# Performance work log

Measured on AMD Instinct MI355X. Metric: run time of the kernel, lower is better.

The kernel has to match this reference:

```python
import jax, jax.numpy as jnp
import numpy as np

GROUP_SIZE = 128
EPS = 1e-6
# AWQ nibble interleave order within each int32
_AWQ_SHIFTS = jnp.array([0, 4, 1, 5, 2, 6, 3, 7], dtype=jnp.uint32) * 4


def dequant_awq(qw, qz, sc, group_size=GROUP_SIZE):
    # qw: (in, out//8) int32, qz: (in//g, out//8) int32, sc: (in//g, out) float
    in_dim = qw.shape[0]
    w4 = ((qw.astype(jnp.uint32)[:, :, None] >> _AWQ_SHIFTS) & 0xF).astype(sc.dtype)
    z4 = ((qz.astype(jnp.uint32)[:, :, None] >> _AWQ_SHIFTS) & 0xF).astype(sc.dtype)
    w4 = w4.reshape(in_dim, -1)                    # (in, out)
    z4 = z4.reshape(qz.shape[0], -1)               # (in//g, out)
    z = jnp.repeat(z4, group_size, axis=0)         # (in, out)
    s = jnp.repeat(sc, group_size, axis=0)         # (in, out)
    return (w4 - z) * s


def rmsnorm(x, w, eps=EPS):
    return x * w * jax.lax.rsqrt(jnp.mean(x * x, axis=-1, keepdims=True) + eps)


def setup_inputs() -> dict:
    key = jax.random.key(0)
    ks = jax.random.split(key, 16)
    H, I, G = 2048, 8192, GROUP_SIZE
    IMAX = 2**31 - 1
    d = {}
    d['x'] = jax.random.normal(ks[0], (2, 2048, H), dtype=jnp.float32)
    d['ln1_w'] = jnp.ones((H,), jnp.float32)
    d['ln2_w'] = jnp.ones((H,), jnp.float32)
    d['qkv_qw'] = jax.random.randint(ks[1], (H, 3 * H // 8), 0, IMAX, dtype=jnp.int32)
    d['qkv_qz'] = jax.random.randint(ks[2], (H // G, 3 * H // 8), 0, IMAX, dtype=jnp.int32)
    d['qkv_sc'] = jax.random.normal(ks[3], (H // G, 3 * H), dtype=jnp.float32) * 0.02
    d['o_qw'] = jax.random.randint(ks[4], (H, H // 8), 0, IMAX, dtype=jnp.int32)
    d['o_qz'] = jax.random.randint(ks[5], (H // G, H // 8), 0, IMAX, dtype=jnp.int32)
    d['o_sc'] = jax.random.normal(ks[6], (H // G, H), dtype=jnp.float32) * 0.02
    d['gu_qw'] = jax.random.randint(ks[7], (H, 2 * I // 8), 0, IMAX, dtype=jnp.int32)
    d['gu_qz'] = jax.random.randint(ks[8], (H // G, 2 * I // 8), 0, IMAX, dtype=jnp.int32)
    d['gu_sc'] = jax.random.normal(ks[9], (H // G, 2 * I), dtype=jnp.float32) * 0.02
    d['dn_qw'] = jax.random.randint(ks[10], (I, H // 8), 0, IMAX, dtype=jnp.int32)
    d['dn_qz'] = jax.random.randint(ks[11], (I // G, H // 8), 0, IMAX, dtype=jnp.int32)
    d['dn_sc'] = jax.random.normal(ks[12], (I // G, H), dtype=jnp.float32) * 0.02
    return d


def reference(x, ln1_w, ln2_w, qkv_qw, qkv_qz, qkv_sc, o_qw, o_qz, o_sc,
              gu_qw, gu_qz, gu_sc, dn_qw, dn_qz, dn_sc):
    H = x.shape[-1]
    # attention-ish block (mock: qkv proj, take q slice, o proj)
    residual = x
    h = rmsnorm(x, ln1_w)
    qkv = h @ dequant_awq(qkv_qw, qkv_qz, qkv_sc)          # (..., 3H)
    q = qkv[..., :H]
    o = q @ dequant_awq(o_qw, o_qz, o_sc)                  # (..., H)
    x = residual + o
    # SwiGLU MLP
    residual = x
    h = rmsnorm(x, ln2_w)
    gate_up = h @ dequant_awq(gu_qw, gu_qz, gu_sc)         # (..., 2I)
    gate, up = jnp.split(gate_up, 2, axis=-1)
    mlp = (jax.nn.silu(gate) * up) @ dequant_awq(dn_qw, dn_qz, dn_sc)
    return residual + mlp
```

## Files before the change

kernel.cpp:

```cpp
#include <hip/hip_runtime.h>
#include <hip/hip_bf16.h>
#include <stdint.h>

typedef __bf16 bf16x8 __attribute__((ext_vector_type(8)));
typedef __bf16 bf16x2 __attribute__((ext_vector_type(2)));
typedef float  f32x4  __attribute__((ext_vector_type(4)));

template <int V> struct ic { static constexpr int value = V; };

__device__ __forceinline__ void gload_lds16(const void* g, void* l) {
  __builtin_amdgcn_global_load_lds(
      (const __attribute__((address_space(1))) void*)g,
      (__attribute__((address_space(3))) void*)l, 16, 0, 0);
}

__global__ __launch_bounds__(256) void rmsnorm_kernel(
    const float* __restrict__ x, const float* __restrict__ w,
    __bf16* __restrict__ out) {
  constexpr int H = 2048;
  const int row = blockIdx.x;
  const int t = threadIdx.x;
  const float4* xr = (const float4*)(x + (size_t)row * H);
  float4 a = xr[t * 2 + 0];
  float4 b = xr[t * 2 + 1];
  float ss = a.x*a.x + a.y*a.y + a.z*a.z + a.w*a.w
           + b.x*b.x + b.y*b.y + b.z*b.z + b.w*b.w;
#pragma unroll
  for (int o = 32; o > 0; o >>= 1) ss += __shfl_xor(ss, o);
  __shared__ float red[4];
  if ((t & 63) == 0) red[t >> 6] = ss;
  __syncthreads();
  float tot = red[0] + red[1] + red[2] + red[3];
  float r = rsqrtf(tot * (1.0f / H) + 1e-6f);
  const float4* wr4 = (const float4*)w;
  float4 wa = wr4[t * 2 + 0];
  float4 wb = wr4[t * 2 + 1];
  bf16x8 ov;
  ov[0] = (__bf16)(a.x * wa.x * r);
  ov[1] = (__bf16)(a.y * wa.y * r);
  ov[2] = (__bf16)(a.z * wa.z * r);
  ov[3] = (__bf16)(a.w * wa.w * r);
  ov[4] = (__bf16)(b.x * wb.x * r);
  ov[5] = (__bf16)(b.y * wb.y * r);
  ov[6] = (__bf16)(b.z * wb.z * r);
  ov[7] = (__bf16)(b.w * wb.w * r);
  *(bf16x8*)(out + (size_t)row * H + (size_t)t * 8) = ov;
}

template <int GU>
__global__ __launch_bounds__(256) void dequant_t_kernel(
    const int* __restrict__ qw, const int* __restrict__ qz,
    const float* __restrict__ sc, __bf16* __restrict__ wt,
    int K, int Cp, int Nfull) {
  const int t = threadIdx.x;
  const int k0 = blockIdx.x * 128 + (t & 63) * 2;
  const int c0 = blockIdx.y * 64 + (t >> 6) * 16;
  const int g = k0 >> 7;
  const uint32_t* qw0 = (const uint32_t*)qw + (size_t)k0 * Cp + c0;
  const uint32_t* qw1 = qw0 + Cp;
  const uint32_t* qzr = (const uint32_t*)qz + (size_t)g * Cp + c0;
  const float* scr = sc + (size_t)g * Nfull + (size_t)c0 * 8;

  uint32_t u0[16], u1[16], z[16];
#pragma unroll
  for (int j = 0; j < 4; j++) {
    *(int4*)(&u0[j*4]) = *(const int4*)(qw0 + j*4);
    *(int4*)(&u1[j*4]) = *(const int4*)(qw1 + j*4);
    *(int4*)(&z[j*4])  = *(const int4*)(qzr + j*4);
  }

#pragma unroll
  for (int i = 0; i < 16; i++) {
#pragma unroll
    for (int s = 0; s < 8; s++) {
      const int sh = ((s >> 1) * 4) + ((s & 1) ? 16 : 0);
      const float zf = (float)((z[i] >> sh) & 15u);
      const float scv = scr[i * 8 + s];
      const float w0 = ((float)((u0[i] >> sh) & 15u) - zf) * scv;
      const float w1 = ((float)((u1[i] >> sh) & 15u) - zf) * scv;
      const int n = (c0 + i) * 8 + s;
      int row;
      if (GU) row = (n < 8192) ? ((n >> 4) * 32 + (n & 15))
                               : (((n - 8192) >> 4) * 32 + 16 + (n & 15));
      else    row = n;
      bf16x2 pv = {(__bf16)w0, (__bf16)w1};
      *(bf16x2*)(wt + (size_t)row * K + k0) = pv;
    }
  }
}

template <int BN, int EPI, int KC>
__global__ __launch_bounds__(512, 2) void gemm8p_kernel(
    const __bf16* __restrict__ A, const __bf16* __restrict__ Bt,
    void* __restrict__ Cv, const float* __restrict__ addend,
    int M, int N) {
  constexpr int NT = KC / 64;
  constexpr int BQ = BN / 64;
  constexpr int NSTRIP = BN / 4;
  constexpr int NI = NSTRIP / 16;

  __shared__ alignas(16) __bf16 As[8 * 4096];
  __shared__ alignas(16) __bf16 Bs[2 * BQ * 4096];

  const int t = threadIdx.x;
  const int w = t >> 6, l = t & 63;
  const int lm = l & 15, kb = l >> 4;
  const int l7 = lm & 7;
  const int wm = w >> 2, wn = w & 3;

  const size_t stat = (size_t)(t >> 3) * KC + (size_t)(((t & 7) ^ ((t >> 3) & 7)) << 3);

  const int nwg = gridDim.x;
  const int bid = blockIdx.x;
  const int swz = (bid & 7) * (nwg >> 3) + (bid >> 3);
  const int nbm = M >> 8;
  const int per_g = nbm * 8;
  const int grp = swz / per_g, v = swz % per_g;
  const int bm0 = (v % nbm) * 256;
  const int bn0 = (grp * 8 + v / nbm) * BN;

  const __bf16* Ab = A + (size_t)bm0 * KC;
  const __bf16* Bb = Bt + (size_t)bn0 * KC;

  const uint32_t gsw0 = (uint32_t)((kb ^ l7) << 4);
  const uint32_t gsw1 = (uint32_t)(((4 + kb) ^ l7) << 4);
  const uint32_t arow = (uint32_t)(wm * 16384 + lm * 128);
  const uint32_t aoff0 = arow + gsw0, aoff1 = arow + gsw1;
  const uint32_t brow = (BN == 256)
      ? (uint32_t)(wn * 8192 + lm * 128)
      : (uint32_t)((wn >> 1) * 8192 + (wn & 1) * 4096 + lm * 128);
  const uint32_t boff0 = brow + gsw0, boff1 = brow + gsw1;
  const char* AsC = (const char*)As;
  const char* BsC = (const char*)Bs;

  f32x4 acc[8][NI] = {};
  bf16x8 af[2][2][2];
  bf16x8 bfr[2][NI][2];

  auto ldAf = [&](int dD, int mi, bf16x8* dst) {
    const uint32_t imA = (uint32_t)((dD * 4 + (mi >> 2)) * 8192 + (mi & 3) * 2048);
    dst[0] = *(const bf16x8*)(AsC + aoff0 + imA);
    dst[1] = *(const bf16x8*)(AsC + aoff1 + imA);
  };
  auto ldBf = [&](int dD) {
#pragma unroll
    for (int ni = 0; ni < NI; ++ni) {
      const uint32_t imB = (uint32_t)(dD * BQ * 8192 + ni * 2048);
      bfr[dD][ni][0] = *(const bf16x8*)(BsC + boff0 + imB);
      bfr[dD][ni][1] = *(const bf16x8*)(BsC + boff1 + imB);
    }
  };
  auto mfma4 = [&](int q, bf16x8 afq[2][2], int dD) {
    __builtin_amdgcn_s_setprio(1);
#pragma unroll
    for (int kk = 0; kk < 2; ++kk)
#pragma unroll
      for (int ni = 0; ni < NI; ++ni)
#pragma unroll
        for (int m2 = 0; m2 < 2; ++m2)
          acc[q * 2 + m2][ni] = __builtin_amdgcn_mfma_f32_16x16x32_bf16(
              afq[m2][kk], bfr[dD][ni][kk], acc[q * 2 + m2][ni], 0, 0, 0);
    __builtin_amdgcn_s_setprio(0);
  };

#pragma unroll
  for (int qa = 0; qa < 4; ++qa)
    gload_lds16(Ab + stat + (size_t)(qa * 64) * KC, As + qa * 4096 + t * 8);
#pragma unroll
  for (int qb = 0; qb < BQ; ++qb)
    gload_lds16(Bb + stat + (size_t)(qb * 64) * KC, Bs + qb * 4096 + t * 8);
#pragma unroll
  for (int qb = 0; qb < BQ; ++qb)
    gload_lds16(Bb + stat + (size_t)(qb * 64) * KC + 64, Bs + (BQ + qb) * 4096 + t * 8);
  gload_lds16(Ab + stat + 64, As + 4 * 4096 + t * 8);
  gload_lds16(Ab + stat + (size_t)128 * KC + 64, As + 6 * 4096 + t * 8);
  if (BN == 256) asm volatile("s_waitcnt vmcnt(6)" ::: "memory");
  else           asm volatile("s_waitcnt vmcnt(4)" ::: "memory");
  __builtin_amdgcn_s_barrier();

  ldAf(0, 0, af[0][0]); ldAf(0, 1, af[0][1]);
  ldBf(0);
  asm volatile("" ::: "memory");

  const __bf16* pA0 = Ab + stat + 128;
  const __bf16* pA1 = Ab + stat + (size_t)64 * KC + 64;
  const __bf16* pA2 = Ab + stat + (size_t)128 * KC + 128;
  const __bf16* pA3 = Ab + stat + (size_t)192 * KC + 64;
  const __bf16* pB0 = Bb + stat + 128;
  const __bf16* pB1 = Bb + stat + (size_t)64 * KC + 128;
  const __bf16* pB2 = Bb + stat + (size_t)128 * KC + 128;
  const __bf16* pB3 = Bb + stat + (size_t)192 * KC + 128;

  auto tile = [&](auto Dc, auto Sc) {
    constexpr int D = decltype(Dc)::value;
    constexpr int STG = decltype(Sc)::value;
    ldAf(D, 2, af[1][0]); ldAf(D, 3, af[1][1]);
    asm volatile("" ::: "memory");
    if (STG >= 1) {
      gload_lds16(pA1, As + ((D ^ 1) * 4 + 1) * 4096 + t * 8);
      gload_lds16(pA3, As + ((D ^ 1) * 4 + 3) * 4096 + t * 8);
    }
    __builtin_amdgcn_s_barrier();
    mfma4(0, af[0], D);
    __builtin_amdgcn_s_barrier();
    ldAf(D, 4, af[0][0]); ldAf(D, 5, af[0][1]);
    asm volatile("" ::: "memory");
    if (STG == 2) {
      gload_lds16(pB0, Bs + (D * BQ + 0) * 4096 + t * 8);
      gload_lds16(pB1, Bs + (D * BQ + 1) * 4096 + t * 8);
    }
    __builtin_amdgcn_s_barrier();
    mfma4(1, af[1], D);
    __builtin_amdgcn_s_barrier();
    ldAf(D, 6, af[1][0]); ldAf(D, 7, af[1][1]);
    asm volatile("" ::: "memory");
    if (STG == 2) {
      if (BN == 256) {
        gload_lds16(pB2, Bs + (D * BQ + 2) * 4096 + t * 8);
        gload_lds16(pB3, Bs + (D * BQ + 3) * 4096 + t * 8);
      } else {
        gload_lds16(pA0, As + (D * 4 + 0) * 4096 + t * 8);
        gload_lds16(pA2, As + (D * 4 + 2) * 4096 + t * 8);
      }
    }
    __builtin_amdgcn_s_barrier();
    mfma4(2, af[0], D);
    __builtin_amdgcn_s_barrier();
    asm volatile("s_waitcnt lgkmcnt(0)" ::: "memory");
    __builtin_amdgcn_sched_barrier(0);
    if (STG == 2)      asm volatile("s_waitcnt vmcnt(4)" ::: "memory");
    else if (STG == 1) asm volatile("s_waitcnt vmcnt(0)" ::: "memory");
    __builtin_amdgcn_s_barrier();
    if (STG >= 1) {
      ldAf(D ^ 1, 0, af[0][0]); ldAf(D ^ 1, 1, af[0][1]);
      ldBf(D ^ 1);
      asm volatile("" ::: "memory");
    }
    if (STG == 2 && BN == 256) {
      gload_lds16(pA0, As + (D * 4 + 0) * 4096 + t * 8);
      gload_lds16(pA2, As + (D * 4 + 2) * 4096 + t * 8);
    }
    __builtin_amdgcn_sched_barrier(0);
    mfma4(3, af[1], D);
    __builtin_amdgcn_s_barrier();
    if (STG == 2) {
      pA0 += 64; pA1 += 64; pA2 += 64; pA3 += 64;
      pB0 += 64; pB1 += 64;
      if (BN == 256) { pB2 += 64; pB3 += 64; }
    }
  };

#pragma unroll 1
  for (int it = 0; it < NT / 2 - 1; ++it) {
    tile(ic<0>{}, ic<2>{});
    tile(ic<1>{}, ic<2>{});
  }
  tile(ic<0>{}, ic<1>{});
  tile(ic<1>{}, ic<0>{});

  const int crow0 = bm0 + wm * 128;
#pragma unroll
  for (int mi = 0; mi < 8; ++mi) {
    if (EPI == 2) {
#pragma unroll
      for (int p = 0; p < NI / 2; ++p) {
        const int ni = p * 2;
        const int col = ((bn0 + wn * 64 + ni * 16) >> 5) * 16 + lm;
#pragma unroll
        for (int r = 0; r < 4; ++r) {
          const int row = crow0 + mi * 16 + kb * 4 + r;
          const float gv = acc[mi][ni][r], uv = acc[mi][ni + 1][r];
          const float av = uv * (gv / (1.0f + __expf(-gv)));
          ((__bf16*)Cv)[(size_t)row * 8192 + col] = (__bf16)av;
        }
      }
    } else {
#pragma unroll
      for (int ni = 0; ni < NI; ++ni) {
        const int col = bn0 + wn * NSTRIP + ni * 16 + lm;
#pragma unroll
        for (int r = 0; r < 4; ++r) {
          const int row = crow0 + mi * 16 + kb * 4 + r;
          const size_t idx = (size_t)row * N + col;
          if (EPI == 0) ((__bf16*)Cv)[idx] = (__bf16)acc[mi][ni][r];
          else          ((float*)Cv)[idx] = addend[idx] + acc[mi][ni][r];
        }
      }
    }
  }
}

extern "C" void kernel_launch(void* const* d_in, const int* in_sizes, int n_in,
                              void* d_out, int out_size, void* d_ws, size_t ws_size,
                              hipStream_t stream) {
  const float* x      = (const float*)d_in[0];
  const float* ln1    = (const float*)d_in[1];
  const float* ln2    = (const float*)d_in[2];
  const int*   qkv_qw = (const int*)d_in[3];
  const int*   qkv_qz = (const int*)d_in[4];
  const float* qkv_sc = (const float*)d_in[5];
  const int*   o_qw   = (const int*)d_in[6];
  const int*   o_qz   = (const int*)d_in[7];
  const float* o_sc   = (const float*)d_in[8];
  const int*   gu_qw  = (const int*)d_in[9];
  const int*   gu_qz  = (const int*)d_in[10];
  const float* gu_sc  = (const float*)d_in[11];
  const int*   dn_qw  = (const int*)d_in[12];
  const int*   dn_qz  = (const int*)d_in[13];
  const float* dn_sc  = (const float*)d_in[14];

  constexpr int M = 4096;

  char* ws = (char*)d_ws;
  __bf16* h   = (__bf16*)(ws + 0);
  __bf16* q   = (__bf16*)(ws + 16777216ULL);
  float*  x2  = (float*)(ws + 33554432ULL);
  __bf16* W   = (__bf16*)(ws + 67108864ULL);
  __bf16* act = (__bf16*)(ws + 134217728ULL);
  __bf16* Wdn = (__bf16*)(ws + 0);

  rmsnorm_kernel<<<dim3(M), dim3(256), 0, stream>>>(x, ln1, h);
  dequant_t_kernel<0><<<dim3(16, 4), dim3(256), 0, stream>>>(qkv_qw, qkv_qz, qkv_sc, W, 2048, 768, 6144);
  gemm8p_kernel<128, 0, 2048><<<dim3(256), dim3(512), 0, stream>>>(h, W, (void*)q, nullptr, M, 2048);
  dequant_t_kernel<0><<<dim3(16, 4), dim3(256), 0, stream>>>(o_qw, o_qz, o_sc, W, 2048, 256, 2048);
  gemm8p_kernel<128, 1, 2048><<<dim3(256), dim3(512), 0, stream>>>(q, W, (void*)x2, x, M, 2048);
  rmsnorm_kernel<<<dim3(M), dim3(256), 0, stream>>>(x2, ln2, h);
  dequant_t_kernel<1><<<dim3(16, 32), dim3(256), 0, stream>>>(gu_qw, gu_qz, gu_sc, W, 2048, 2048, 16384);
  gemm8p_kernel<256, 2, 2048><<<dim3(1024), dim3(512), 0, stream>>>(h, W, (void*)act, nullptr, M, 16384);
  dequant_t_kernel<0><<<dim3(64, 4), dim3(256), 0, stream>>>(dn_qw, dn_qz, dn_sc, Wdn, 8192, 256, 2048);
  gemm8p_kernel<128, 1, 8192><<<dim3(256), dim3(512), 0, stream>>>(act, Wdn, d_out, x2, M, 2048);
}
```

Measured before the change: 513.4 us.

## Switch GEMMs to 32x32x16 MFMA tiles with reworked LDS fragment pipeline

Replaces the 16x16x32 bf16 MFMA inner product with 32x32x16 MFMAs, so each wave keeps 4xNI2 32x32 accumulators and loads larger A/B fragments from LDS. The per-tile pipeline is restructured into either four or two phases (NPH template parameter) depending on tile width, and the gate/up weight interleave changes from 16- to 32-column blocks to match the new epilogue layout. The aim is fewer LDS reads per FLOP and fewer MFMA issues. In exchange it raises register pressure and changes the barrier and wait schedule.

```diff
diff --git a/kernel.cpp b/kernel.cpp
--- a/kernel.cpp
+++ b/kernel.cpp
@@ -4,7 +4,7 @@
 
 typedef __bf16 bf16x8 __attribute__((ext_vector_type(8)));
 typedef __bf16 bf16x2 __attribute__((ext_vector_type(2)));
-typedef float  f32x4  __attribute__((ext_vector_type(4)));
+typedef float  f32x16 __attribute__((ext_vector_type(16)));
 
 template <int V> struct ic { static constexpr int value = V; };
 
@@ -80,8 +80,8 @@
       const float w1 = ((float)((u1[i] >> sh) & 15u) - zf) * scv;
       const int n = (c0 + i) * 8 + s;
       int row;
-      if (GU) row = (n < 8192) ? ((n >> 4) * 32 + (n & 15))
-                               : (((n - 8192) >> 4) * 32 + 16 + (n & 15));
+      if (GU) row = (n < 8192) ? ((n >> 5) * 64 + (n & 31))
+                               : (((n - 8192) >> 5) * 64 + 32 + (n & 31));
       else    row = n;
       bf16x2 pv = {(__bf16)w0, (__bf16)w1};
       *(bf16x2*)(wt + (size_t)row * K + k0) = pv;
@@ -89,23 +89,22 @@
   }
 }
 
-template <int BN, int EPI, int KC>
-__global__ __launch_bounds__(512, 2) void gemm8p_kernel(
+template <int BN, int EPI, int KC, int NPH>
+__global__ __launch_bounds__(512, 2) void gemm32_kernel(
     const __bf16* __restrict__ A, const __bf16* __restrict__ Bt,
     void* __restrict__ Cv, const float* __restrict__ addend,
     int M, int N) {
   constexpr int NT = KC / 64;
   constexpr int BQ = BN / 64;
-  constexpr int NSTRIP = BN / 4;
-  constexpr int NI = NSTRIP / 16;
+  constexpr int NI2 = BN / 128;
+  constexpr int KSP = 4 / NPH;
 
   __shared__ alignas(16) __bf16 As[8 * 4096];
   __shared__ alignas(16) __bf16 Bs[2 * BQ * 4096];
 
   const int t = threadIdx.x;
   const int w = t >> 6, l = t & 63;
-  const int lm = l & 15, kb = l >> 4;
-  const int l7 = lm & 7;
+  const int l31 = l & 31, h = l >> 5, l7 = l & 7;
   const int wm = w >> 2, wn = w & 3;
 
   const size_t stat = (size_t)(t >> 3) * KC + (size_t)(((t & 7) ^ ((t >> 3) & 7)) << 3);
@@ -122,44 +121,48 @@
   const __bf16* Ab = A + (size_t)bm0 * KC;
   const __bf16* Bb = Bt + (size_t)bn0 * KC;
 
-  const uint32_t gsw0 = (uint32_t)((kb ^ l7) << 4);
-  const uint32_t gsw1 = (uint32_t)(((4 + kb) ^ l7) << 4);
-  const uint32_t arow = (uint32_t)(wm * 16384 + lm * 128);
-  const uint32_t aoff0 = arow + gsw0, aoff1 = arow + gsw1;
-  const uint32_t brow = (BN == 256)
-      ? (uint32_t)(wn * 8192 + lm * 128)
-      : (uint32_t)((wn >> 1) * 8192 + (wn & 1) * 4096 + lm * 128);
-  const uint32_t boff0 = brow + gsw0, boff1 = brow + gsw1;
+  uint32_t Abase[4], Bbase[4];
+#pragma unroll
+  for (int q = 0; q < 4; ++q) {
+    const uint32_t sw = (uint32_t)(((2 * q + h) ^ l7) << 4);
+    Abase[q] = (uint32_t)(wm * 16384 + l31 * 128) + sw;
+    Bbase[q] = (uint32_t)((BN == 256 ? wn * 8192 : (wn >> 1) * 8192 + (wn & 1) * 4096)
+                          + l31 * 128) + sw;
+  }
   const char* AsC = (const char*)As;
   const char* BsC = (const char*)Bs;
 
-  f32x4 acc[8][NI] = {};
-  bf16x8 af[2][2][2];
-  bf16x8 bfr[2][NI][2];
-
-  auto ldAf = [&](int dD, int mi, bf16x8* dst) {
-    const uint32_t imA = (uint32_t)((dD * 4 + (mi >> 2)) * 8192 + (mi & 3) * 2048);
-    dst[0] = *(const bf16x8*)(AsC + aoff0 + imA);
-    dst[1] = *(const bf16x8*)(AsC + aoff1 + imA);
+  f32x16 acc[4][NI2] = {};
+  bf16x8 af2[2][4 * KSP];
+  bf16x8 bfr[2][NI2][4];
+
+  auto ldAset = [&](int P, int Dd, int qb) {
+#pragma unroll
+    for (int s = 0; s < KSP; ++s)
+#pragma unroll
+      for (int mi = 0; mi < 4; ++mi)
+        af2[P][mi * KSP + s] = *(const bf16x8*)
+            (AsC + Abase[qb + s] + (uint32_t)(Dd * 32768 + mi * 4096));
   };
-  auto ldBf = [&](int dD) {
-#pragma unroll
-    for (int ni = 0; ni < NI; ++ni) {
-      const uint32_t imB = (uint32_t)(dD * BQ * 8192 + ni * 2048);
-      bfr[dD][ni][0] = *(const bf16x8*)(BsC + boff0 + imB);
-      bfr[dD][ni][1] = *(const bf16x8*)(BsC + boff1 + imB);
-    }
+  auto ldB = [&](int Dp) {
+#pragma unroll
+    for (int ni = 0; ni < NI2; ++ni)
+#pragma unroll
+      for (int q = 0; q < 4; ++q)
+        bfr[Dp][ni][q] = *(const bf16x8*)
+            (BsC + Bbase[q] + (uint32_t)(Dp * BQ * 8192 + ni * 4096));
   };
-  auto mfma4 = [&](int q, bf16x8 afq[2][2], int dD) {
+  auto mfmaP = [&](int p, int Dp) {
     __builtin_amdgcn_s_setprio(1);
 #pragma unroll
-    for (int kk = 0; kk < 2; ++kk)
-#pragma unroll
-      for (int ni = 0; ni < NI; ++ni)
-#pragma unroll
-        for (int m2 = 0; m2 < 2; ++m2)
-          acc[q * 2 + m2][ni] = __builtin_amdgcn_mfma_f32_16x16x32_bf16(
-              afq[m2][kk], bfr[dD][ni][kk], acc[q * 2 + m2][ni], 0, 0, 0);
+    for (int s = 0; s < KSP; ++s)
+#pragma unroll
+      for (int mi = 0; mi < 4; ++mi)
+#pragma unroll
+        for (int ni = 0; ni < NI2; ++ni)
+          acc[mi][ni] = __builtin_amdgcn_mfma_f32_32x32x16_bf16(
+              af2[p & 1][mi * KSP + s], bfr[Dp][ni][p * KSP + s],
+              acc[mi][ni], 0, 0, 0);
     __builtin_amdgcn_s_setprio(0);
   };
 
@@ -178,8 +181,8 @@
   else           asm volatile("s_waitcnt vmcnt(4)" ::: "memory");
   __builtin_amdgcn_s_barrier();
 
-  ldAf(0, 0, af[0][0]); ldAf(0, 1, af[0][1]);
-  ldBf(0);
+  ldAset(0, 0, 0);
+  ldB(0);
   asm volatile("" ::: "memory");
 
   const __bf16* pA0 = Ab + stat + 128;
@@ -194,55 +197,85 @@
   auto tile = [&](auto Dc, auto Sc) {
     constexpr int D = decltype(Dc)::value;
     constexpr int STG = decltype(Sc)::value;
-    ldAf(D, 2, af[1][0]); ldAf(D, 3, af[1][1]);
-    asm volatile("" ::: "memory");
-    if (STG >= 1) {
-      gload_lds16(pA1, As + ((D ^ 1) * 4 + 1) * 4096 + t * 8);
-      gload_lds16(pA3, As + ((D ^ 1) * 4 + 3) * 4096 + t * 8);
-    }
-    __builtin_amdgcn_s_barrier();
-    mfma4(0, af[0], D);
-    __builtin_amdgcn_s_barrier();
-    ldAf(D, 4, af[0][0]); ldAf(D, 5, af[0][1]);
-    asm volatile("" ::: "memory");
-    if (STG == 2) {
-      gload_lds16(pB0, Bs + (D * BQ + 0) * 4096 + t * 8);
-      gload_lds16(pB1, Bs + (D * BQ + 1) * 4096 + t * 8);
-    }
-    __builtin_amdgcn_s_barrier();
-    mfma4(1, af[1], D);
-    __builtin_amdgcn_s_barrier();
-    ldAf(D, 6, af[1][0]); ldAf(D, 7, af[1][1]);
-    asm volatile("" ::: "memory");
-    if (STG == 2) {
-      if (BN == 256) {
+    if constexpr (NPH == 4) {
+      ldAset(1, D, 1);
+      asm volatile("" ::: "memory");
+      if (STG >= 1) {
+        gload_lds16(pA1, As + ((D ^ 1) * 4 + 1) * 4096 + t * 8);
+        gload_lds16(pA3, As + ((D ^ 1) * 4 + 3) * 4096 + t * 8);
+      }
+      __builtin_amdgcn_s_barrier();
+      mfmaP(0, D);
+      __builtin_amdgcn_s_barrier();
+      ldAset(0, D, 2);
+      asm volatile("" ::: "memory");
+      if (STG == 2) {
+        gload_lds16(pB0, Bs + (D * BQ + 0) * 4096 + t * 8);
+        gload_lds16(pB1, Bs + (D * BQ + 1) * 4096 + t * 8);
+      }
+      __builtin_amdgcn_s_barrier();
+      mfmaP(1, D);
+      __builtin_amdgcn_s_barrier();
+      ldAset(1, D, 3);
+      asm volatile("" ::: "memory");
+      if (STG == 2) {
         gload_lds16(pB2, Bs + (D * BQ + 2) * 4096 + t * 8);
         gload_lds16(pB3, Bs + (D * BQ + 3) * 4096 + t * 8);
-      } else {
+      }
+      __builtin_amdgcn_s_barrier();
+      mfmaP(2, D);
+      __builtin_amdgcn_s_barrier();
+      asm volatile("s_waitcnt lgkmcnt(0)" ::: "memory");
+      __builtin_amdgcn_sched_barrier(0);
+      if (STG == 2)      asm volatile("s_waitcnt vmcnt(4)" ::: "memory");
+      else if (STG == 1) asm volatile("s_waitcnt vmcnt(0)" ::: "memory");
+      __builtin_amdgcn_s_barrier();
+      if (STG >= 1) {
+        ldAset(0, D ^ 1, 0);
+        ldB(D ^ 1);
+        asm volatile("" ::: "memory");
+      }
+      if (STG == 2) {
         gload_lds16(pA0, As + (D * 4 + 0) * 4096 + t * 8);
         gload_lds16(pA2, As + (D * 4 + 2) * 4096 + t * 8);
       }
+      __builtin_amdgcn_sched_barrier(0);
+      mfmaP(3, D);
+      asm volatile("s_waitcnt lgkmcnt(0)" ::: "memory");
+      __builtin_amdgcn_s_barrier();
+    } else {
+      ldAset(1, D, 2);
+      asm volatile("" ::: "memory");
+      if (STG >= 1) {
+        gload_lds16(pA1, As + ((D ^ 1) * 4 + 1) * 4096 + t * 8);
+        gload_lds16(pA3, As + ((D ^ 1) * 4 + 3) * 4096 + t * 8);
+      }
+      if (STG == 2) {
+        gload_lds16(pB0, Bs + (D * BQ + 0) * 4096 + t * 8);
+        gload_lds16(pB1, Bs + (D * BQ + 1) * 4096 + t * 8);
+      }
+      __builtin_amdgcn_s_barrier();
+      mfmaP(0, D);
+      __builtin_amdgcn_s_barrier();
+      asm volatile("s_waitcnt lgkmcnt(0)" ::: "memory");
+      __builtin_amdgcn_sched_barrier(0);
+      if (STG == 2)      asm volatile("s_waitcnt vmcnt(2)" ::: "memory");
+      else if (STG == 1) asm volatile("s_waitcnt vmcnt(0)" ::: "memory");
+      __builtin_amdgcn_s_barrier();
+      if (STG >= 1) {
+        ldAset(0, D ^ 1, 0);
+        ldB(D ^ 1);
+        asm volatile("" ::: "memory");
+      }
+      if (STG == 2) {
+        gload_lds16(pA0, As + (D * 4 + 0) * 4096 + t * 8);
+        gload_lds16(pA2, As + (D * 4 + 2) * 4096 + t * 8);
+      }
+      __builtin_amdgcn_sched_barrier(0);
+      mfmaP(1, D);
+      asm volatile("s_waitcnt lgkmcnt(0)" ::: "memory");
+      __builtin_amdgcn_s_barrier();
     }
-    __builtin_amdgcn_s_barrier();
-    mfma4(2, af[0], D);
-    __builtin_amdgcn_s_barrier();
-    asm volatile("s_waitcnt lgkmcnt(0)" ::: "memory");
-    __builtin_amdgcn_sched_barrier(0);
-    if (STG == 2)      asm volatile("s_waitcnt vmcnt(4)" ::: "memory");
-    else if (STG == 1) asm volatile("s_waitcnt vmcnt(0)" ::: "memory");
-    __builtin_amdgcn_s_barrier();
-    if (STG >= 1) {
-      ldAf(D ^ 1, 0, af[0][0]); ldAf(D ^ 1, 1, af[0][1]);
-      ldBf(D ^ 1);
-      asm volatile("" ::: "memory");
-    }
-    if (STG == 2 && BN == 256) {
-      gload_lds16(pA0, As + (D * 4 + 0) * 4096 + t * 8);
-      gload_lds16(pA2, As + (D * 4 + 2) * 4096 + t * 8);
-    }
-    __builtin_amdgcn_sched_barrier(0);
-    mfma4(3, af[1], D);
-    __builtin_amdgcn_s_barrier();
     if (STG == 2) {
       pA0 += 64; pA1 += 64; pA2 += 64; pA3 += 64;
       pB0 += 64; pB1 += 64;
@@ -260,27 +293,23 @@
 
   const int crow0 = bm0 + wm * 128;
 #pragma unroll
-  for (int mi = 0; mi < 8; ++mi) {
+  for (int mi = 0; mi < 4; ++mi) {
     if (EPI == 2) {
-#pragma unroll
-      for (int p = 0; p < NI / 2; ++p) {
-        const int ni = p * 2;
-        const int col = ((bn0 + wn * 64 + ni * 16) >> 5) * 16 + lm;
-#pragma unroll
-        for (int r = 0; r < 4; ++r) {
-          const int row = crow0 + mi * 16 + kb * 4 + r;
-          const float gv = acc[mi][ni][r], uv = acc[mi][ni + 1][r];
-          const float av = uv * (gv / (1.0f + __expf(-gv)));
-          ((__bf16*)Cv)[(size_t)row * 8192 + col] = (__bf16)av;
-        }
+      const int colb = (bn0 >> 1) + wn * 32 + l31;
+#pragma unroll
+      for (int r = 0; r < 16; ++r) {
+        const int row = crow0 + mi * 32 + (r & 3) + 8 * (r >> 2) + 4 * h;
+        const float gv = acc[mi][0][r], uv = acc[mi][1][r];
+        const float av = uv * (gv / (1.0f + __expf(-gv)));
+        ((__bf16*)Cv)[(size_t)row * 8192 + colb] = (__bf16)av;
       }
     } else {
 #pragma unroll
-      for (int ni = 0; ni < NI; ++ni) {
-        const int col = bn0 + wn * NSTRIP + ni * 16 + lm;
-#pragma unroll
-        for (int r = 0; r < 4; ++r) {
-          const int row = crow0 + mi * 16 + kb * 4 + r;
+      for (int ni = 0; ni < NI2; ++ni) {
+        const int col = bn0 + wn * (BN / 4) + ni * 32 + l31;
+#pragma unroll
+        for (int r = 0; r < 16; ++r) {
+          const int row = crow0 + mi * 32 + (r & 3) + 8 * (r >> 2) + 4 * h;
           const size_t idx = (size_t)row * N + col;
           if (EPI == 0) ((__bf16*)Cv)[idx] = (__bf16)acc[mi][ni][r];
           else          ((float*)Cv)[idx] = addend[idx] + acc[mi][ni][r];
@@ -321,12 +350,12 @@
 
   rmsnorm_kernel<<<dim3(M), dim3(256), 0, stream>>>(x, ln1, h);
   dequant_t_kernel<0><<<dim3(16, 4), dim3(256), 0, stream>>>(qkv_qw, qkv_qz, qkv_sc, W, 2048, 768, 6144);
-  gemm8p_kernel<128, 0, 2048><<<dim3(256), dim3(512), 0, stream>>>(h, W, (void*)q, nullptr, M, 2048);
+  gemm32_kernel<128, 0, 2048, 2><<<dim3(256), dim3(512), 0, stream>>>(h, W, (void*)q, nullptr, M, 2048);
   dequant_t_kernel<0><<<dim3(16, 4), dim3(256), 0, stream>>>(o_qw, o_qz, o_sc, W, 2048, 256, 2048);
-  gemm8p_kernel<128, 1, 2048><<<dim3(256), dim3(512), 0, stream>>>(q, W, (void*)x2, x, M, 2048);
+  gemm32_kernel<128, 1, 2048, 2><<<dim3(256), dim3(512), 0, stream>>>(q, W, (void*)x2, x, M, 2048);
   rmsnorm_kernel<<<dim3(M), dim3(256), 0, stream>>>(x2, ln2, h);
   dequant_t_kernel<1><<<dim3(16, 32), dim3(256), 0, stream>>>(gu_qw, gu_qz, gu_sc, W, 2048, 2048, 16384);
-  gemm8p_kernel<256, 2, 2048><<<dim3(1024), dim3(512), 0, stream>>>(h, W, (void*)act, nullptr, M, 16384);
+  gemm32_kernel<256, 2, 2048, 4><<<dim3(1024), dim3(512), 0, stream>>>(h, W, (void*)act, nullptr, M, 16384);
   dequant_t_kernel<0><<<dim3(64, 4), dim3(256), 0, stream>>>(dn_qw, dn_qz, dn_sc, Wdn, 8192, 256, 2048);
-  gemm8p_kernel<128, 1, 8192><<<dim3(256), dim3(512), 0, stream>>>(act, Wdn, d_out, x2, M, 2048);
-}
+  gemm32_kernel<128, 1, 8192, 2><<<dim3(256), dim3(512), 0, stream>>>(act, Wdn, d_out, x2, M, 2048);
+}
```

After: 554.9 us. 8.1% more time.

## Add two-phase tile schedule for BN=128 GEMMs with larger MFMA batches

Applied to the files above, without the earlier changes.

Adds an NPH template parameter: BN=128 GEMMs now run a two-phase per-tile schedule, each phase issuing MFMAs over four A fragments instead of two, with fewer barriers and reordered global-to-LDS loads. BN=256 keeps the four-phase schedule but drops the BN==128 branches. The goal is to cut barrier and sync overhead and give longer MFMA runs for the narrow-N GEMMs. The cost is more A-fragment registers live at once and less interleaving of loads with compute.

```diff
diff --git a/kernel.cpp b/kernel.cpp
--- a/kernel.cpp
+++ b/kernel.cpp
@@ -89,7 +89,7 @@
   }
 }
 
-template <int BN, int EPI, int KC>
+template <int BN, int EPI, int KC, int NPH>
 __global__ __launch_bounds__(512, 2) void gemm8p_kernel(
     const __bf16* __restrict__ A, const __bf16* __restrict__ Bt,
     void* __restrict__ Cv, const float* __restrict__ addend,
@@ -98,6 +98,7 @@
   constexpr int BQ = BN / 64;
   constexpr int NSTRIP = BN / 4;
   constexpr int NI = NSTRIP / 16;
+  constexpr int MIP = (NPH == 4) ? 2 : 4;
 
   __shared__ alignas(16) __bf16 As[8 * 4096];
   __shared__ alignas(16) __bf16 Bs[2 * BQ * 4096];
@@ -134,7 +135,7 @@
   const char* BsC = (const char*)Bs;
 
   f32x4 acc[8][NI] = {};
-  bf16x8 af[2][2][2];
+  bf16x8 af[2][MIP][2];
   bf16x8 bfr[2][NI][2];
 
   auto ldAf = [&](int dD, int mi, bf16x8* dst) {
@@ -160,6 +161,18 @@
         for (int m2 = 0; m2 < 2; ++m2)
           acc[q * 2 + m2][ni] = __builtin_amdgcn_mfma_f32_16x16x32_bf16(
               afq[m2][kk], bfr[dD][ni][kk], acc[q * 2 + m2][ni], 0, 0, 0);
+    __builtin_amdgcn_s_setprio(0);
+  };
+  auto mfmaH = [&](int S, int dD) {
+    __builtin_amdgcn_s_setprio(1);
+#pragma unroll
+    for (int kk = 0; kk < 2; ++kk)
+#pragma unroll
+      for (int ni = 0; ni < NI; ++ni)
+#pragma unroll
+        for (int m2 = 0; m2 < 4; ++m2)
+          acc[S * 4 + m2][ni] = __builtin_amdgcn_mfma_f32_16x16x32_bf16(
+              af[S][m2][kk], bfr[dD][ni][kk], acc[S * 4 + m2][ni], 0, 0, 0);
     __builtin_amdgcn_s_setprio(0);
   };
 
@@ -178,9 +191,13 @@
   else           asm volatile("s_waitcnt vmcnt(4)" ::: "memory");
   __builtin_amdgcn_s_barrier();
 
-  ldAf(0, 0, af[0][0]); ldAf(0, 1, af[0][1]);
+  if constexpr (NPH == 4) {
+    ldAf(0, 0, af[0][0]); ldAf(0, 1, af[0][1]);
+  } else {
+#pragma unroll
+    for (int m2 = 0; m2 < 4; ++m2) ldAf(0, m2, af[0][m2]);
+  }
   ldBf(0);
-  asm volatile("" ::: "memory");
 
   const __bf16* pA0 = Ab + stat + 128;
   const __bf16* pA1 = Ab + stat + (size_t)64 * KC + 64;
@@ -194,55 +211,81 @@
   auto tile = [&](auto Dc, auto Sc) {
     constexpr int D = decltype(Dc)::value;
     constexpr int STG = decltype(Sc)::value;
-    ldAf(D, 2, af[1][0]); ldAf(D, 3, af[1][1]);
-    asm volatile("" ::: "memory");
-    if (STG >= 1) {
-      gload_lds16(pA1, As + ((D ^ 1) * 4 + 1) * 4096 + t * 8);
-      gload_lds16(pA3, As + ((D ^ 1) * 4 + 3) * 4096 + t * 8);
-    }
-    __builtin_amdgcn_s_barrier();
-    mfma4(0, af[0], D);
-    __builtin_amdgcn_s_barrier();
-    ldAf(D, 4, af[0][0]); ldAf(D, 5, af[0][1]);
-    asm volatile("" ::: "memory");
-    if (STG == 2) {
-      gload_lds16(pB0, Bs + (D * BQ + 0) * 4096 + t * 8);
-      gload_lds16(pB1, Bs + (D * BQ + 1) * 4096 + t * 8);
-    }
-    __builtin_amdgcn_s_barrier();
-    mfma4(1, af[1], D);
-    __builtin_amdgcn_s_barrier();
-    ldAf(D, 6, af[1][0]); ldAf(D, 7, af[1][1]);
-    asm volatile("" ::: "memory");
-    if (STG == 2) {
-      if (BN == 256) {
+    if constexpr (NPH == 4) {
+      ldAf(D, 2, af[1][0]); ldAf(D, 3, af[1][1]);
+      asm volatile("" ::: "memory");
+      if (STG >= 1) {
+        gload_lds16(pA1, As + ((D ^ 1) * 4 + 1) * 4096 + t * 8);
+        gload_lds16(pA3, As + ((D ^ 1) * 4 + 3) * 4096 + t * 8);
+      }
+      __builtin_amdgcn_s_barrier();
+      mfma4(0, af[0], D);
+      __builtin_amdgcn_s_barrier();
+      ldAf(D, 4, af[0][0]); ldAf(D, 5, af[0][1]);
+      asm volatile("" ::: "memory");
+      if (STG == 2) {
+        gload_lds16(pB0, Bs + (D * BQ + 0) * 4096 + t * 8);
+        gload_lds16(pB1, Bs + (D * BQ + 1) * 4096 + t * 8);
+      }
+      __builtin_amdgcn_s_barrier();
+      mfma4(1, af[1], D);
+      __builtin_amdgcn_s_barrier();
+      ldAf(D, 6, af[1][0]); ldAf(D, 7, af[1][1]);
+      asm volatile("" ::: "memory");
+      if (STG == 2) {
         gload_lds16(pB2, Bs + (D * BQ + 2) * 4096 + t * 8);
         gload_lds16(pB3, Bs + (D * BQ + 3) * 4096 + t * 8);
-      } else {
+      }
+      __builtin_amdgcn_s_barrier();
+      mfma4(2, af[0], D);
+      __builtin_amdgcn_s_barrier();
+      asm volatile("s_waitcnt lgkmcnt(0)" ::: "memory");
+      __builtin_amdgcn_sched_barrier(0);
+      if (STG == 2)      asm volatile("s_waitcnt vmcnt(4)" ::: "memory");
+      else if (STG == 1) asm volatile("s_waitcnt vmcnt(0)" ::: "memory");
+      __builtin_amdgcn_s_barrier();
+      if (STG == 2) {
         gload_lds16(pA0, As + (D * 4 + 0) * 4096 + t * 8);
         gload_lds16(pA2, As + (D * 4 + 2) * 4096 + t * 8);
       }
-    }
-    __builtin_amdgcn_s_barrier();
-    mfma4(2, af[0], D);
-    __builtin_amdgcn_s_barrier();
-    asm volatile("s_waitcnt lgkmcnt(0)" ::: "memory");
-    __builtin_amdgcn_sched_barrier(0);
-    if (STG == 2)      asm volatile("s_waitcnt vmcnt(4)" ::: "memory");
-    else if (STG == 1) asm volatile("s_waitcnt vmcnt(0)" ::: "memory");
-    __builtin_amdgcn_s_barrier();
-    if (STG >= 1) {
-      ldAf(D ^ 1, 0, af[0][0]); ldAf(D ^ 1, 1, af[0][1]);
-      ldBf(D ^ 1);
+      if (STG >= 1) {
+        ldAf(D ^ 1, 0, af[0][0]); ldAf(D ^ 1, 1, af[0][1]);
+        ldBf(D ^ 1);
+      }
+      mfma4(3, af[1], D);
+      __builtin_amdgcn_s_barrier();
+    } else {
+#pragma unroll
+      for (int m2 = 0; m2 < 4; ++m2) ldAf(D, 4 + m2, af[1][m2]);
       asm volatile("" ::: "memory");
-    }
-    if (STG == 2 && BN == 256) {
-      gload_lds16(pA0, As + (D * 4 + 0) * 4096 + t * 8);
-      gload_lds16(pA2, As + (D * 4 + 2) * 4096 + t * 8);
-    }
-    __builtin_amdgcn_sched_barrier(0);
-    mfma4(3, af[1], D);
-    __builtin_amdgcn_s_barrier();
+      if (STG >= 1) {
+        gload_lds16(pA1, As + ((D ^ 1) * 4 + 1) * 4096 + t * 8);
+        gload_lds16(pA3, As + ((D ^ 1) * 4 + 3) * 4096 + t * 8);
+      }
+      if (STG == 2)
+        gload_lds16(pB0, Bs + (D * BQ + 0) * 4096 + t * 8);
+      __builtin_amdgcn_s_barrier();
+      mfmaH(0, D);
+      __builtin_amdgcn_s_barrier();
+      asm volatile("s_waitcnt lgkmcnt(0)" ::: "memory");
+      __builtin_amdgcn_sched_barrier(0);
+      if (STG == 2)      asm volatile("s_waitcnt vmcnt(1)" ::: "memory");
+      else if (STG == 1) asm volatile("s_waitcnt vmcnt(0)" ::: "memory");
+      __builtin_amdgcn_s_barrier();
+      if (STG >= 1) {
+#pragma unroll
+        for (int m2 = 0; m2 < 4; ++m2) ldAf(D ^ 1, m2, af[0][m2]);
+        ldBf(D ^ 1);
+      }
+      if (STG == 2) {
+        gload_lds16(pB1, Bs + (D * BQ + 1) * 4096 + t * 8);
+        gload_lds16(pA0, As + (D * 4 + 0) * 4096 + t * 8);
+        gload_lds16(pA2, As + (D * 4 + 2) * 4096 + t * 8);
+      }
+      mfmaH(1, D);
+      asm volatile("s_waitcnt lgkmcnt(0)" ::: "memory");
+      __builtin_amdgcn_s_barrier();
+    }
     if (STG == 2) {
       pA0 += 64; pA1 += 64; pA2 += 64; pA3 += 64;
       pB0 += 64; pB1 += 64;
@@ -321,12 +364,12 @@
 
   rmsnorm_kernel<<<dim3(M), dim3(256), 0, stream>>>(x, ln1, h);
   dequant_t_kernel<0><<<dim3(16, 4), dim3(256), 0, stream>>>(qkv_qw, qkv_qz, qkv_sc, W, 2048, 768, 6144);
-  gemm8p_kernel<128, 0, 2048><<<dim3(256), dim3(512), 0, stream>>>(h, W, (void*)q, nullptr, M, 2048);
+  gemm8p_kernel<128, 0, 2048, 2><<<dim3(256), dim3(512), 0, stream>>>(h, W, (void*)q, nullptr, M, 2048);
   dequant_t_kernel<0><<<dim3(16, 4), dim3(256), 0, stream>>>(o_qw, o_qz, o_sc, W, 2048, 256, 2048);
-  gemm8p_kernel<128, 1, 2048><<<dim3(256), dim3(512), 0, stream>>>(q, W, (void*)x2, x, M, 2048);
+  gemm8p_kernel<128, 1, 2048, 2><<<dim3(256), dim3(512), 0, stream>>>(q, W, (void*)x2, x, M, 2048);
   rmsnorm_kernel<<<dim3(M), dim3(256), 0, stream>>>(x2, ln2, h);
   dequant_t_kernel<1><<<dim3(16, 32), dim3(256), 0, stream>>>(gu_qw, gu_qz, gu_sc, W, 2048, 2048, 16384);
-  gemm8p_kernel<256, 2, 2048><<<dim3(1024), dim3(512), 0, stream>>>(h, W, (void*)act, nullptr, M, 16384);
+  gemm8p_kernel<256, 2, 2048, 4><<<dim3(1024), dim3(512), 0, stream>>>(h, W, (void*)act, nullptr, M, 16384);
   dequant_t_kernel<0><<<dim3(64, 4), dim3(256), 0, stream>>>(dn_qw, dn_qz, dn_sc, Wdn, 8192, 256, 2048);
-  gemm8p_kernel<128, 1, 8192><<<dim3(256), dim3(512), 0, stream>>>(act, Wdn, d_out, x2, M, 2048);
-}
+  gemm8p_kernel<128, 1, 8192, 2><<<dim3(256), dim3(512), 0, stream>>>(act, Wdn, d_out, x2, M, 2048);
+}
```

After: 530.4 us. +3.3%, slower.

## Fuse AWQ dequantization into gate-up GEMM with in-kernel B unpacking

Applied to the files above, without the earlier changes.

Replaces the separate gate/up dequant kernel plus bf16 GEMM with one kernel that loads packed int4 weights, zeros and scales from global memory and unpacks them into swizzled LDS tiles inside the main loop. It overlaps the unpack with MFMA phases and applies the SiLU-gate epilogue directly. This removes writing and rereading the 64MB bf16 weight matrix and one launch. In exchange every workgroup redoes the dequant ALU work for its N-slice, and register pressure rises under launch_bounds(512,2).

```diff
diff --git a/kernel.cpp b/kernel.cpp
--- a/kernel.cpp
+++ b/kernel.cpp
@@ -3,6 +3,7 @@
 #include <stdint.h>
 
 typedef __bf16 bf16x8 __attribute__((ext_vector_type(8)));
+typedef __bf16 bf16x4 __attribute__((ext_vector_type(4)));
 typedef __bf16 bf16x2 __attribute__((ext_vector_type(2)));
 typedef float  f32x4  __attribute__((ext_vector_type(4)));
 
@@ -234,7 +235,6 @@
     if (STG >= 1) {
       ldAf(D ^ 1, 0, af[0][0]); ldAf(D ^ 1, 1, af[0][1]);
       ldBf(D ^ 1);
-      asm volatile("" ::: "memory");
     }
     if (STG == 2 && BN == 256) {
       gload_lds16(pA0, As + (D * 4 + 0) * 4096 + t * 8);
@@ -285,6 +285,216 @@
           if (EPI == 0) ((__bf16*)Cv)[idx] = (__bf16)acc[mi][ni][r];
           else          ((float*)Cv)[idx] = addend[idx] + acc[mi][ni][r];
         }
+      }
+    }
+  }
+}
+
+__global__ __launch_bounds__(512, 2) void gemm_gu_kernel(
+    const __bf16* __restrict__ A, const int* __restrict__ qw,
+    const int* __restrict__ qz, const float* __restrict__ sc,
+    __bf16* __restrict__ act, int M) {
+  constexpr int KC = 2048, NT = 32, BQ = 4, NI = 4, Cp = 2048;
+
+  __shared__ alignas(16) __bf16 As[8 * 4096];
+  __shared__ alignas(16) __bf16 Bs[2 * BQ * 4096];
+
+  const int t = threadIdx.x;
+  const int w = t >> 6, l = t & 63;
+  const int lm = l & 15, kb = l >> 4;
+  const int l7 = lm & 7;
+  const int wm = w >> 2, wn = w & 3;
+
+  const size_t stat = (size_t)(t >> 3) * KC + (size_t)(((t & 7) ^ ((t >> 3) & 7)) << 3);
+
+  const int nwg = gridDim.x;
+  const int bid = blockIdx.x;
+  const int swz = (bid & 7) * (nwg >> 3) + (bid >> 3);
+  const int nbm = M >> 8;
+  const int per_g = nbm * 8;
+  const int grp = swz / per_g, v = swz % per_g;
+  const int bm0 = (v % nbm) * 256;
+  const int bn0 = (grp * 8 + v / nbm) * 256;
+
+  const __bf16* Ab = A + (size_t)bm0 * KC;
+
+  const int cl = t & 31;
+  const int kslab = t >> 5;
+  const int k0 = kslab * 4;
+  const int clg = (cl < 16) ? cl : (cl - 16);
+  const int rl0 = ((clg >> 1) << 5) + ((clg & 1) << 3) + ((cl < 16) ? 0 : 16);
+  const int c = (cl < 16) ? ((bn0 >> 4) + cl) : (1024 + (bn0 >> 4) + cl - 16);
+  const uint32_t G = (uint32_t)(kslab >> 1);
+  const uint32_t wOff = (uint32_t)(((rl0 >> 6) << 13) + ((rl0 & 63) << 7) + ((kslab & 1) << 3));
+  const uint32_t rot = (uint32_t)(t & 7);
+  const uint32_t* qcol = (const uint32_t*)qw + c;
+  const uint32_t* qzc  = (const uint32_t*)qz + c;
+  const float*    scc  = sc + (size_t)c * 8;
+
+  const uint32_t gsw0 = (uint32_t)((kb ^ l7) << 4);
+  const uint32_t gsw1 = (uint32_t)(((4 + kb) ^ l7) << 4);
+  const uint32_t arow = (uint32_t)(wm * 16384 + lm * 128);
+  const uint32_t aoff0 = arow + gsw0, aoff1 = arow + gsw1;
+  const uint32_t boff0 = (uint32_t)(wn * 8192 + lm * 128) + gsw0;
+  const uint32_t boff1 = (uint32_t)(wn * 8192 + lm * 128) + gsw1;
+  const char* AsC = (const char*)As;
+  const char* BsC = (const char*)Bs;
+  char* BsW = (char*)Bs;
+
+  f32x4 acc[8][NI] = {};
+  bf16x8 af[2][2][2];
+  bf16x8 bfr[NI][2];
+  uint32_t bq[4];
+  float scf[8];
+  uint32_t qzv = 0;
+
+  auto ldAf = [&](int dD, int mi, bf16x8* dst) {
+    const uint32_t imA = (uint32_t)((dD * 4 + (mi >> 2)) * 8192 + (mi & 3) * 2048);
+    dst[0] = *(const bf16x8*)(AsC + aoff0 + imA);
+    dst[1] = *(const bf16x8*)(AsC + aoff1 + imA);
+  };
+  auto ldBf = [&](int dD) {
+#pragma unroll
+    for (int ni = 0; ni < NI; ++ni) {
+      const uint32_t imB = (uint32_t)(dD * 32768 + ni * 2048);
+      bfr[ni][0] = *(const bf16x8*)(BsC + boff0 + imB);
+      bfr[ni][1] = *(const bf16x8*)(BsC + boff1 + imB);
+    }
+  };
+  auto mfma4 = [&](int q, bf16x8 afq[2][2]) {
+    __builtin_amdgcn_s_setprio(1);
+#pragma unroll
+    for (int kk = 0; kk < 2; ++kk)
+#pragma unroll
+      for (int ni = 0; ni < NI; ++ni)
+#pragma unroll
+        for (int m2 = 0; m2 < 2; ++m2)
+          acc[q * 2 + m2][ni] = __builtin_amdgcn_mfma_f32_16x16x32_bf16(
+              afq[m2][kk], bfr[ni][kk], acc[q * 2 + m2][ni], 0, 0, 0);
+    __builtin_amdgcn_s_setprio(0);
+  };
+  auto unpackWrite = [&](int Dd, int sp0, int sp1) {
+#pragma unroll
+    for (int sp = sp0; sp < sp1; ++sp) {
+      const uint32_t s = (uint32_t)((sp + rot) & 7);
+      const uint32_t sh = ((s >> 1) << 2) | ((s & 1) << 4);
+      const float zf = (float)((qzv >> sh) & 15u);
+      const float scv = scf[sp];
+      bf16x4 vv;
+#pragma unroll
+      for (int i = 0; i < 4; ++i)
+        vv[i] = (__bf16)(((float)((bq[i] >> sh) & 15u) - zf) * scv);
+      *(bf16x4*)(BsW + Dd * 32768 + wOff + (s << 7) + ((G ^ s) << 4)) = vv;
+    }
+  };
+
+#pragma unroll
+  for (int qa = 0; qa < 4; ++qa)
+    gload_lds16(Ab + stat + (size_t)(qa * 64) * KC, As + qa * 4096 + t * 8);
+  gload_lds16(Ab + stat + 64, As + 4 * 4096 + t * 8);
+  gload_lds16(Ab + stat + (size_t)128 * KC + 64, As + 6 * 4096 + t * 8);
+  qzv = qzc[0];
+#pragma unroll
+  for (int sp = 0; sp < 8; ++sp) scf[sp] = scc[(sp + rot) & 7];
+#pragma unroll
+  for (int i = 0; i < 4; ++i) bq[i] = qcol[(size_t)(k0 + i) * Cp];
+  unpackWrite(0, 0, 8);
+#pragma unroll
+  for (int i = 0; i < 4; ++i) bq[i] = qcol[(size_t)(64 + k0 + i) * Cp];
+  unpackWrite(1, 0, 8);
+#pragma unroll
+  for (int i = 0; i < 4; ++i) bq[i] = qcol[(size_t)(128 + k0 + i) * Cp];
+  qzv = qzc[2048];
+#pragma unroll
+  for (int sp = 0; sp < 8; ++sp) scf[sp] = scc[16384 + ((sp + rot) & 7)];
+  asm volatile("s_waitcnt lgkmcnt(0)" ::: "memory");
+  __builtin_amdgcn_s_barrier();
+  ldAf(0, 0, af[0][0]); ldAf(0, 1, af[0][1]);
+  asm volatile("" ::: "memory");
+
+  const __bf16* pA0 = Ab + stat + 128;
+  const __bf16* pA1 = Ab + stat + (size_t)64 * KC + 64;
+  const __bf16* pA2 = Ab + stat + (size_t)128 * KC + 128;
+  const __bf16* pA3 = Ab + stat + (size_t)192 * KC + 64;
+  const uint32_t* pBq = qcol + (size_t)(k0 + 192) * Cp;
+  const float* scd = scc + 16384;
+  const uint32_t* qzd = qzc + 2048;
+
+  auto tile = [&](auto Dc, auto Sc) {
+    constexpr int D = decltype(Dc)::value;
+    constexpr int STG = decltype(Sc)::value;
+    ldBf(D);
+    ldAf(D, 2, af[1][0]); ldAf(D, 3, af[1][1]);
+    asm volatile("" ::: "memory");
+    if (STG >= 1) {
+      gload_lds16(pA1, As + ((D ^ 1) * 4 + 1) * 4096 + t * 8);
+      gload_lds16(pA3, As + ((D ^ 1) * 4 + 3) * 4096 + t * 8);
+    }
+    __builtin_amdgcn_s_barrier();
+    mfma4(0, af[0]);
+    __builtin_amdgcn_s_barrier();
+    ldAf(D, 4, af[0][0]); ldAf(D, 5, af[0][1]);
+    asm volatile("" ::: "memory");
+    if (STG >= 2) unpackWrite(D, 0, 4);
+    __builtin_amdgcn_s_barrier();
+    mfma4(1, af[1]);
+    __builtin_amdgcn_s_barrier();
+    ldAf(D, 6, af[1][0]); ldAf(D, 7, af[1][1]);
+    asm volatile("" ::: "memory");
+    if (STG >= 2) unpackWrite(D, 4, 8);
+    if (STG == 2) {
+#pragma unroll
+      for (int i = 0; i < 4; ++i) bq[i] = pBq[(size_t)i * Cp];
+    }
+    __builtin_amdgcn_s_barrier();
+    mfma4(2, af[0]);
+    __builtin_amdgcn_s_barrier();
+    asm volatile("s_waitcnt lgkmcnt(0)" ::: "memory");
+    __builtin_amdgcn_sched_barrier(0);
+    if (STG == 2)      asm volatile("s_waitcnt vmcnt(4)" ::: "memory");
+    else if (STG == 3 || STG == 1) asm volatile("s_waitcnt vmcnt(0)" ::: "memory");
+    __builtin_amdgcn_s_barrier();
+    if (STG == 2) {
+      if (D == 1) { scd += 16384; qzd += 2048; }
+      qzv = qzd[0];
+#pragma unroll
+      for (int sp = 0; sp < 8; ++sp) scf[sp] = scd[(sp + rot) & 7];
+    }
+    if (STG >= 1) { ldAf(D ^ 1, 0, af[0][0]); ldAf(D ^ 1, 1, af[0][1]); }
+    if (STG >= 2) {
+      gload_lds16(pA0, As + (D * 4 + 0) * 4096 + t * 8);
+      gload_lds16(pA2, As + (D * 4 + 2) * 4096 + t * 8);
+    }
+    __builtin_amdgcn_sched_barrier(0);
+    mfma4(3, af[1]);
+    __builtin_amdgcn_s_barrier();
+    if (STG >= 2) { pA0 += 64; pA1 += 64; pA2 += 64; pA3 += 64; }
+    if (STG == 2) pBq += (size_t)64 * Cp;
+  };
+
+#pragma unroll 1
+  for (int it = 0; it < 14; ++it) {
+    tile(ic<0>{}, ic<2>{});
+    tile(ic<1>{}, ic<2>{});
+  }
+  tile(ic<0>{}, ic<2>{});
+  tile(ic<1>{}, ic<3>{});
+  tile(ic<0>{}, ic<1>{});
+  tile(ic<1>{}, ic<0>{});
+
+  const int crow0 = bm0 + wm * 128;
+#pragma unroll
+  for (int mi = 0; mi < 8; ++mi) {
+#pragma unroll
+    for (int p = 0; p < 2; ++p) {
+      const int ni = p * 2;
+      const int col = ((bn0 + wn * 64 + ni * 16) >> 5) * 16 + lm;
+#pragma unroll
+      for (int r = 0; r < 4; ++r) {
+        const int row = crow0 + mi * 16 + kb * 4 + r;
+        const float gv = acc[mi][ni][r], uv = acc[mi][ni + 1][r];
+        const float av = uv * (gv / (1.0f + __expf(-gv)));
+        act[(size_t)row * 8192 + col] = (__bf16)av;
       }
     }
   }
@@ -325,8 +535,7 @@
   dequant_t_kernel<0><<<dim3(16, 4), dim3(256), 0, stream>>>(o_qw, o_qz, o_sc, W, 2048, 256, 2048);
   gemm8p_kernel<128, 1, 2048><<<dim3(256), dim3(512), 0, stream>>>(q, W, (void*)x2, x, M, 2048);
   rmsnorm_kernel<<<dim3(M), dim3(256), 0, stream>>>(x2, ln2, h);
-  dequant_t_kernel<1><<<dim3(16, 32), dim3(256), 0, stream>>>(gu_qw, gu_qz, gu_sc, W, 2048, 2048, 16384);
-  gemm8p_kernel<256, 2, 2048><<<dim3(1024), dim3(512), 0, stream>>>(h, W, (void*)act, nullptr, M, 16384);
+  gemm_gu_kernel<<<dim3(1024), dim3(512), 0, stream>>>(h, gu_qw, gu_qz, gu_sc, act, M);
   dequant_t_kernel<0><<<dim3(64, 4), dim3(256), 0, stream>>>(dn_qw, dn_qz, dn_sc, Wdn, 8192, 256, 2048);
   gemm8p_kernel<128, 1, 8192><<<dim3(256), dim3(512), 0, stream>>>(act, Wdn, d_out, x2, M, 2048);
 }
```

Result: slower. 1.474 ms (+187.1%).
